# Kernel optimization log

Measured on AMD Instinct MI355X. Metric: run time of the kernel, lower is better.

Reference implementation:

```python
import jax, jax.numpy as jnp
import numpy as np

E = 128  # embedding_dim
C = 32   # per-head dim
H = 4    # heads
L = 256  # seq_len
N = 1    # batch


def layer_norm(x, gamma, beta, eps=1e-5):
    mu = jnp.mean(x, axis=-1, keepdims=True)
    var = jnp.mean((x - mu) ** 2, axis=-1, keepdims=True)
    return (x - mu) * jax.lax.rsqrt(var + eps) * gamma + beta


def setup_inputs() -> dict:
    key = jax.random.key(0)
    ks = jax.random.split(key, 12)
    s = E ** -0.5
    return {
        "pair_rep": jax.random.normal(ks[0], (N, L, L, E), dtype=jnp.float32),
        "mask": jax.random.normal(ks[1], (N, L, L), dtype=jnp.float32) * 0.1,
        "gamma": jnp.ones((E,), dtype=jnp.float32),
        "beta": jnp.zeros((E,), dtype=jnp.float32),
        "Wq": jax.random.normal(ks[2], (E, C * H), dtype=jnp.float32) * s,
        "Wk": jax.random.normal(ks[3], (E, C * H), dtype=jnp.float32) * s,
        "Wv": jax.random.normal(ks[4], (E, C * H), dtype=jnp.float32) * s,
        "Wb": jax.random.normal(ks[5], (E, H), dtype=jnp.float32) * s,
        "Wfu": jax.random.normal(ks[6], (E, C * H), dtype=jnp.float32) * s,
        "bfu": jnp.zeros((C * H,), dtype=jnp.float32),
        "Wo": jax.random.normal(ks[7], (C * H, E), dtype=jnp.float32) * (C * H) ** -0.5,
        "bo": jnp.zeros((E,), dtype=jnp.float32),
    }


def reference(pair_rep, mask, gamma, beta, Wq, Wk, Wv, Wb, Wfu, bfu, Wo, bo):
    n, s, _, _ = pair_rep.shape
    x = layer_norm(pair_rep, gamma, beta)  # [n,s,s,E]
    q = (x @ Wq).reshape(n, s, s, H, C) * (C ** -0.5)
    k = (x @ Wk).reshape(n, s, s, H, C)
    v = (x @ Wv).reshape(n, s, s, H, C)
    # faithful to original einsum: keys carry the q index, queries the v index
    dpa = jnp.einsum('nsqhc,nsvhc->nsqvh', k, q)  # [n,s,q,v,h]
    dpa = dpa + mask[:, None, :, :, None]
    pair_bias = x @ Wb  # [n,s,s,H]
    attn = jax.nn.softmax(dpa + pair_bias[:, None], axis=3)
    out = jnp.einsum('nsqvh,nsvhc->nsqhc', attn, v)  # [n,s,q,h,c]
    fu = jax.nn.sigmoid(x @ Wfu + bfu).reshape(n, s, s, H, C)
    out = out * fu
    out = out.reshape(n, s, s, H * C) @ Wo + bo
    return out
```

## Files before the change

kernel.cpp:

```cpp
#include <hip/hip_runtime.h>
#include <math.h>

#define L 256
#define E 128
#define H 4
#define C 32
#define P (L*L)

typedef __bf16 bf16;
typedef __bf16 bf16x8 __attribute__((ext_vector_type(8)));
typedef __bf16 bf16x4 __attribute__((ext_vector_type(4)));
typedef float  f32x4  __attribute__((ext_vector_type(4)));

#define MFMA(a,b,c) __builtin_amdgcn_mfma_f32_16x16x32_bf16((a),(b),(c),0,0,0)

__global__ __launch_bounds__(256) void k_prep(
    const float* __restrict__ Wq, const float* __restrict__ Wk,
    const float* __restrict__ Wv, const float* __restrict__ Wfu,
    const float* __restrict__ Wo, const float* __restrict__ Wb,
    bf16* __restrict__ WF, bf16* __restrict__ WoF, bf16* __restrict__ WbF)
{
  const int b = blockIdx.x;
  const int lane = threadIdx.x & 63, wv = threadIdx.x >> 6;
  const int g = lane >> 4, l15 = lane & 15;
  if (b < 40) {
    const int m = b >> 3;
    const int f = (b & 7) * 4 + wv;
    const float* W = (m==0)?Wq:(m==1)?Wk:(m==2)?Wv:(m==3)?Wfu:Wo;
    bf16* dst = (m < 4) ? (WF + (size_t)m * 16384) : WoF;
    const float sc = (m == 0) ? 0.17677669529663689f : 1.0f;
    const int mt = f >> 2, kt = f & 3;
    const int row = 16*mt + l15, k0 = 32*kt + 8*g;
    bf16x8 o;
    #pragma unroll
    for (int j = 0; j < 8; ++j) o[j] = (bf16)(W[(size_t)(k0+j)*128 + row] * sc);
    *(bf16x8*)(dst + ((size_t)f*64 + lane)*8) = o;
  } else {
    const int kt = wv, k0 = 32*kt + 8*g;
    bf16x8 o;
    #pragma unroll
    for (int j = 0; j < 8; ++j)
      o[j] = (l15 < 4) ? (bf16)Wb[(size_t)(k0+j)*4 + l15] : (bf16)0.0f;
    *(bf16x8*)(WbF + ((size_t)kt*64 + lane)*8) = o;
  }
}

__global__ __launch_bounds__(512) void k_ln_proj(
    const float* __restrict__ pr, const float* __restrict__ gamma,
    const float* __restrict__ beta, const float* __restrict__ bfu,
    const bf16* __restrict__ WF, const bf16* __restrict__ WbF,
    bf16* __restrict__ qb, bf16* __restrict__ kb, bf16* __restrict__ vb,
    bf16* __restrict__ gfb, float* __restrict__ pbo)
{
  __shared__ bf16 xs[64 * 136];
  __shared__ bf16 stag[4][16 * 136];
  const int tid = threadIdx.x;
  const int base = blockIdx.x * 64;
  const int w = tid >> 6, lane = tid & 63, g = lane >> 4, l15 = lane & 15;
  const int m = w & 3, half = w >> 2;

  const bf16* WFw = WF + (size_t)m * 16384 + (size_t)half * 8192;
  f32x4 af[16];
  #pragma unroll
  for (int f = 0; f < 16; ++f)
    af[f] = *(const f32x4*)(WFw + ((size_t)f*64 + lane)*8);

  {
    const int pl = tid >> 3, sub = tid & 7;
    const float4* src = (const float4*)(pr + (size_t)(base + pl) * 128 + sub * 16);
    float4 r[4];
    float s = 0.f, ss = 0.f;
    #pragma unroll
    for (int j = 0; j < 4; ++j) {
      r[j] = src[j];
      s  += r[j].x + r[j].y + r[j].z + r[j].w;
      ss += r[j].x*r[j].x + r[j].y*r[j].y + r[j].z*r[j].z + r[j].w*r[j].w;
    }
    s  += __shfl_xor(s, 1, 8);  s  += __shfl_xor(s, 2, 8);  s  += __shfl_xor(s, 4, 8);
    ss += __shfl_xor(ss, 1, 8); ss += __shfl_xor(ss, 2, 8); ss += __shfl_xor(ss, 4, 8);
    const float mu   = s * 0.0078125f;
    const float var  = ss * 0.0078125f - mu * mu;
    const float rstd = rsqrtf(var + 1e-5f);
    const float4* g4 = (const float4*)(gamma + sub * 16);
    const float4* b4 = (const float4*)(beta + sub * 16);
    bf16* xr = xs + pl * 136 + sub * 16;
    #pragma unroll
    for (int i = 0; i < 2; ++i) {
      float4 r0 = r[2*i], r1 = r[2*i+1];
      float4 gg0 = g4[2*i], gg1 = g4[2*i+1], bb0 = b4[2*i], bb1 = b4[2*i+1];
      bf16x8 o;
      o[0] = (bf16)((r0.x - mu) * rstd * gg0.x + bb0.x);
      o[1] = (bf16)((r0.y - mu) * rstd * gg0.y + bb0.y);
      o[2] = (bf16)((r0.z - mu) * rstd * gg0.z + bb0.z);
      o[3] = (bf16)((r0.w - mu) * rstd * gg0.w + bb0.w);
      o[4] = (bf16)((r1.x - mu) * rstd * gg1.x + bb1.x);
      o[5] = (bf16)((r1.y - mu) * rstd * gg1.y + bb1.y);
      o[6] = (bf16)((r1.z - mu) * rstd * gg1.z + bb1.z);
      o[7] = (bf16)((r1.w - mu) * rstd * gg1.w + bb1.w);
      *(bf16x8*)(xr + 8 * i) = o;
    }
  }

  #pragma unroll
  for (int f = 0; f < 16; ++f)
    asm volatile("" : "+v"(af[f]));

  __syncthreads();

  const f32x4 z = {0.f, 0.f, 0.f, 0.f};

  if (w < 4) {
    f32x4 acc = z;
    #pragma unroll
    for (int kt = 0; kt < 4; ++kt) {
      bf16x8 a = *(const bf16x8*)(WbF + ((size_t)kt*64 + lane)*8);
      bf16x8 b = *(const bf16x8*)(xs + (16*w + l15)*136 + 32*kt + 8*g);
      acc = MFMA(a, b, acc);
    }
    if (g == 0)
      *(float4*)(pbo + (size_t)(base + 16*w + l15)*4) =
          make_float4(acc[0], acc[1], acc[2], acc[3]);
  }

  bf16* stw = stag[m];
  bf16* dst = (m == 0) ? qb : (m == 1) ? kb : (m == 2) ? vb : gfb;

  for (int nt = 0; nt < 4; ++nt) {
    bf16x8 bfr[4];
    #pragma unroll
    for (int kt = 0; kt < 4; ++kt)
      bfr[kt] = *(const bf16x8*)(xs + (16*nt + l15)*136 + 32*kt + 8*g);
    f32x4 acc[4];
    #pragma unroll
    for (int mtl = 0; mtl < 4; ++mtl) acc[mtl] = z;
    #pragma unroll
    for (int kt = 0; kt < 4; ++kt)
      #pragma unroll
      for (int mtl = 0; mtl < 4; ++mtl)
        acc[mtl] = MFMA(__builtin_bit_cast(bf16x8, af[mtl*4 + kt]), bfr[kt], acc[mtl]);

    #pragma unroll
    for (int mtl = 0; mtl < 4; ++mtl) {
      const int col = half*64 + 16*mtl + 4*g;
      f32x4 vv = acc[mtl];
      if (m == 3) {
        float4 bb = *(const float4*)(bfu + col);
        vv[0] = 1.f / (1.f + __expf(-(vv[0] + bb.x)));
        vv[1] = 1.f / (1.f + __expf(-(vv[1] + bb.y)));
        vv[2] = 1.f / (1.f + __expf(-(vv[2] + bb.z)));
        vv[3] = 1.f / (1.f + __expf(-(vv[3] + bb.w)));
      }
      bf16x4 o;
      o[0] = (bf16)vv[0]; o[1] = (bf16)vv[1]; o[2] = (bf16)vv[2]; o[3] = (bf16)vv[3];
      *(bf16x4*)(stw + l15*136 + col) = o;
    }

    #pragma unroll
    for (int i = 0; i < 2; ++i) {
      const int flat = i*512 + lane*8;
      const int p = flat >> 6, cf = half*64 + (flat & 63);
      bf16x8 val = *(const bf16x8*)(stw + p*136 + cf);
      *(bf16x8*)(dst + ((size_t)(base + 16*nt + p))*128 + cf) = val;
    }
  }
}

__global__ __launch_bounds__(256) void k_bias(
    const float* __restrict__ mask, const float* __restrict__ pb,
    bf16* __restrict__ T5)
{
  const int q = blockIdx.x;
  const int v = threadIdx.x;
  const size_t qv = (size_t)q*256 + v;
  const float m = mask[qv];
  float4 p = *(const float4*)(pb + qv*4);
  T5[qv]            = (bf16)(m + p.x);
  T5[qv +   65536]  = (bf16)(m + p.y);
  T5[qv + 2*65536]  = (bf16)(m + p.z);
  T5[qv + 3*65536]  = (bf16)(m + p.w);
}

__global__ __launch_bounds__(512) void k_attn(
    const bf16* __restrict__ qb, const bf16* __restrict__ kb,
    const bf16* __restrict__ vb, const bf16* __restrict__ T5,
    bf16* __restrict__ aob)
{
  __shared__ bf16 qs[256 * 40];
  __shared__ bf16 vT[32 * 264];
  const int tid = threadIdx.x;
  const int s = blockIdx.x >> 2, h = blockIdx.x & 3;
  const int rb = s * 256;
  const int hc = 32 * h;
  const bf16* T5h = T5 + (size_t)h * 65536;

  const int w = tid >> 6, lane = tid & 63, g = lane >> 4, l15 = lane & 15;

  #pragma unroll
  for (int i = 0; i < 2; ++i) {
    const int flat = i*4096 + tid*8;
    const int pos = flat >> 5, cc = flat & 31;
    const int slot = (pos & 0xE3) | ((pos & 0x04) << 2) | ((pos & 0x18) >> 1);
    bf16x8 qv = *(const bf16x8*)(qb + ((size_t)rb + pos)*128 + hc + cc);
    *(bf16x8*)(qs + slot*40 + cc) = qv;
    bf16x8 vv = *(const bf16x8*)(vb + ((size_t)rb + pos)*128 + hc + cc);
    #pragma unroll
    for (int j = 0; j < 8; ++j) {
      const int row = cc + j;
      const int a = row >> 3;
      const int X = (a << 5) | ((a >> 1) << 4);
      vT[row*264 + (pos ^ X)] = vv[j];
    }
  }

  bf16x8 bq0 = *(const bf16x8*)(kb + ((size_t)rb + w*32 +      l15)*128 + hc + 8*g);
  bf16x8 bq1 = *(const bf16x8*)(kb + ((size_t)rb + w*32 + 16 + l15)*128 + hc + 8*g);

  __syncthreads();

  bf16x8 av[2][8];
  #pragma unroll
  for (int mt = 0; mt < 2; ++mt) {
    const int row = 16*mt + l15;
    const int a = row >> 3;
    const int X = (a << 5) | ((a >> 1) << 4);
    #pragma unroll
    for (int kt = 0; kt < 8; ++kt)
      av[mt][kt] = *(const bf16x8*)(vT + row*264 + ((32*kt + 8*g) ^ X));
  }

  const f32x4 z = {0.f, 0.f, 0.f, 0.f};

  #pragma unroll
  for (int qt = 0; qt < 2; ++qt) {
    const int q = w*32 + qt*16 + l15;
    const bf16x8 bq = qt ? bq1 : bq0;
    const bf16* Trow = T5h + (size_t)q * 256 + 8*g;
    f32x4 o0a = z, o0b = z, o1a = z, o1b = z;
    float rs = 0.f;
    #pragma unroll
    for (int kt = 0; kt < 8; ++kt) {
      bf16x8 a0 = *(const bf16x8*)(qs + (16*(2*kt + 0) + l15)*40 + 8*g);
      bf16x8 a1 = *(const bf16x8*)(qs + (16*(2*kt + 1) + l15)*40 + 8*g);
      f32x4 s0 = MFMA(a0, bq, z);
      f32x4 s1 = MFMA(a1, bq, z);
      bf16x4 b0 = *(const bf16x4*)(Trow + 32*kt);
      bf16x4 b1 = *(const bf16x4*)(Trow + 32*kt + 4);
      bf16x8 pf;
      #pragma unroll
      for (int r = 0; r < 4; ++r) {
        float e0 = __expf(s0[r] + (float)b0[r]);
        float e1 = __expf(s1[r] + (float)b1[r]);
        pf[r]     = (bf16)e0;
        pf[4 + r] = (bf16)e1;
        rs += e0 + e1;
      }
      if (kt & 1) {
        o0b = MFMA(av[0][kt], pf, o0b);
        o1b = MFMA(av[1][kt], pf, o1b);
      } else {
        o0a = MFMA(av[0][kt], pf, o0a);
        o1a = MFMA(av[1][kt], pf, o1a);
      }
    }
    rs += __shfl_xor(rs, 16);
    rs += __shfl_xor(rs, 32);
    const float inv = 1.f / rs;
    bf16x4 p0, p1;
    #pragma unroll
    for (int r = 0; r < 4; ++r) {
      p0[r] = (bf16)((o0a[r] + o0b[r]) * inv);
      p1[r] = (bf16)((o1a[r] + o1b[r]) * inv);
    }
    bf16* dst = aob + ((size_t)rb + q)*128 + hc;
    *(bf16x4*)(dst + 4*g)      = p0;
    *(bf16x4*)(dst + 16 + 4*g) = p1;
  }
}

__global__ __launch_bounds__(512) void k_gate_out(
    const bf16* __restrict__ aob, const bf16* __restrict__ gfb,
    const bf16* __restrict__ WoF, const float* __restrict__ bo,
    float* __restrict__ out)
{
  __shared__ bf16 gs[64 * 136];
  const int tid = threadIdx.x;
  const int base = blockIdx.x * 64;
  const int w = tid >> 6, lane = tid & 63, g = lane >> 4, l15 = lane & 15;

  f32x4 wf[4];
  #pragma unroll
  for (int kt = 0; kt < 4; ++kt)
    wf[kt] = *(const f32x4*)(WoF + ((size_t)(w*4 + kt)*64 + lane)*8);

  #pragma unroll
  for (int i = 0; i < 2; ++i) {
    const int flat = i*4096 + tid*8;
    const int pos = flat >> 7, c = flat & 127;
    const size_t off = (size_t)(base + pos)*128 + c;
    bf16x8 a = *(const bf16x8*)(aob + off);
    bf16x8 f = *(const bf16x8*)(gfb + off);
    bf16x8 o;
    #pragma unroll
    for (int j = 0; j < 8; ++j) o[j] = (bf16)((float)a[j] * (float)f[j]);
    *(bf16x8*)(gs + pos*136 + c) = o;
  }

  #pragma unroll
  for (int kt = 0; kt < 4; ++kt)
    asm volatile("" : "+v"(wf[kt]));

  __syncthreads();

  const f32x4 z = {0.f, 0.f, 0.f, 0.f};
  const int col = 16*w + 4*g;
  const float4 bb = *(const float4*)(bo + col);

  for (int nt = 0; nt < 4; ++nt) {
    bf16x8 bfr[4];
    #pragma unroll
    for (int kt = 0; kt < 4; ++kt)
      bfr[kt] = *(const bf16x8*)(gs + (16*nt + l15)*136 + 32*kt + 8*g);
    f32x4 a0 = z;
    #pragma unroll
    for (int kt = 0; kt < 4; ++kt)
      a0 = MFMA(__builtin_bit_cast(bf16x8, wf[kt]), bfr[kt], a0);
    const int pos = base + 16*nt + l15;
    *(float4*)(out + (size_t)pos*128 + col) =
        make_float4(a0[0] + bb.x, a0[1] + bb.y, a0[2] + bb.z, a0[3] + bb.w);
  }
}

extern "C" void kernel_launch(void* const* d_in, const int* in_sizes, int n_in,
                              void* d_out, int out_size, void* d_ws, size_t ws_size,
                              hipStream_t stream) {
  const float* pr    = (const float*)d_in[0];
  const float* mask  = (const float*)d_in[1];
  const float* gamma = (const float*)d_in[2];
  const float* beta  = (const float*)d_in[3];
  const float* Wq    = (const float*)d_in[4];
  const float* Wk    = (const float*)d_in[5];
  const float* Wv    = (const float*)d_in[6];
  const float* Wb    = (const float*)d_in[7];
  const float* Wfu   = (const float*)d_in[8];
  const float* bfu   = (const float*)d_in[9];
  const float* Wo    = (const float*)d_in[10];
  const float* bo    = (const float*)d_in[11];
  float* out = (float*)d_out;

  bf16* qb  = (bf16*)d_ws;
  bf16* kb  = qb  + (size_t)P * 128;
  bf16* vb  = kb  + (size_t)P * 128;
  bf16* gfb = vb  + (size_t)P * 128;
  bf16* aob = gfb + (size_t)P * 128;
  bf16* T5  = aob + (size_t)P * 128;
  bf16* WF  = T5  + (size_t)H * P;
  bf16* WoF = WF  + 4 * 16384;
  bf16* WbF = WoF + 16384;
  float* pb = (float*)(WbF + 2048);

  k_prep<<<41, 256, 0, stream>>>(Wq, Wk, Wv, Wfu, Wo, Wb, WF, WoF, WbF);
  k_ln_proj<<<1024, 512, 0, stream>>>(pr, gamma, beta, bfu, WF, WbF,
                                      qb, kb, vb, gfb, pb);
  k_bias<<<256, 256, 0, stream>>>(mask, pb, T5);
  k_attn<<<1024, 512, 0, stream>>>(qb, kb, vb, T5, aob);
  k_gate_out<<<1024, 512, 0, stream>>>(aob, gfb, WoF, bo, out);
}
```

Baseline: 168.0 us.

## Fuse mask-bias add into projection kernel and stage attention output via LDS

```diff
diff --git a/kernel.cpp b/kernel.cpp
--- a/kernel.cpp
+++ b/kernel.cpp
@@ -49,8 +49,9 @@
     const float* __restrict__ pr, const float* __restrict__ gamma,
     const float* __restrict__ beta, const float* __restrict__ bfu,
     const bf16* __restrict__ WF, const bf16* __restrict__ WbF,
+    const float* __restrict__ mask,
     bf16* __restrict__ qb, bf16* __restrict__ kb, bf16* __restrict__ vb,
-    bf16* __restrict__ gfb, float* __restrict__ pbo)
+    bf16* __restrict__ gfb, bf16* __restrict__ T5)
 {
   __shared__ bf16 xs[64 * 136];
   __shared__ bf16 stag[4][16 * 136];
@@ -117,9 +118,14 @@
       bf16x8 b = *(const bf16x8*)(xs + (16*w + l15)*136 + 32*kt + 8*g);
       acc = MFMA(a, b, acc);
     }
-    if (g == 0)
-      *(float4*)(pbo + (size_t)(base + 16*w + l15)*4) =
-          make_float4(acc[0], acc[1], acc[2], acc[3]);
+    if (g == 0) {
+      const int pos = base + 16*w + l15;
+      const float mv = mask[pos];
+      T5[pos]            = (bf16)(mv + acc[0]);
+      T5[pos +   65536]  = (bf16)(mv + acc[1]);
+      T5[pos + 2*65536]  = (bf16)(mv + acc[2]);
+      T5[pos + 3*65536]  = (bf16)(mv + acc[3]);
+    }
   }
 
   bf16* stw = stag[m];
@@ -165,21 +171,6 @@
   }
 }
 
-__global__ __launch_bounds__(256) void k_bias(
-    const float* __restrict__ mask, const float* __restrict__ pb,
-    bf16* __restrict__ T5)
-{
-  const int q = blockIdx.x;
-  const int v = threadIdx.x;
-  const size_t qv = (size_t)q*256 + v;
-  const float m = mask[qv];
-  float4 p = *(const float4*)(pb + qv*4);
-  T5[qv]            = (bf16)(m + p.x);
-  T5[qv +   65536]  = (bf16)(m + p.y);
-  T5[qv + 2*65536]  = (bf16)(m + p.z);
-  T5[qv + 3*65536]  = (bf16)(m + p.w);
-}
-
 __global__ __launch_bounds__(512) void k_attn(
     const bf16* __restrict__ qb, const bf16* __restrict__ kb,
     const bf16* __restrict__ vb, const bf16* __restrict__ T5,
@@ -227,6 +218,9 @@
     for (int kt = 0; kt < 8; ++kt)
       av[mt][kt] = *(const bf16x8*)(vT + row*264 + ((32*kt + 8*g) ^ X));
   }
+
+  __syncthreads();
+  bf16* aost = vT;
 
   const f32x4 z = {0.f, 0.f, 0.f, 0.f};
 
@@ -271,9 +265,20 @@
       p0[r] = (bf16)((o0a[r] + o0b[r]) * inv);
       p1[r] = (bf16)((o1a[r] + o1b[r]) * inv);
     }
-    bf16* dst = aob + ((size_t)rb + q)*128 + hc;
+    bf16* dst = aost + (size_t)q * 32;
     *(bf16x4*)(dst + 4*g)      = p0;
     *(bf16x4*)(dst + 16 + 4*g) = p1;
+  }
+
+  __syncthreads();
+
+  bf16* aoh = aob + (size_t)h * P * 32;
+  #pragma unroll
+  for (int i = 0; i < 2; ++i) {
+    const int flat = i*4096 + tid*8;
+    const int pos = flat >> 5, cc = flat & 31;
+    *(bf16x8*)(aoh + ((size_t)rb + pos)*32 + cc) =
+        *(const bf16x8*)(aost + pos*32 + cc);
   }
 }
 
@@ -295,10 +300,9 @@
   #pragma unroll
   for (int i = 0; i < 2; ++i) {
     const int flat = i*4096 + tid*8;
-    const int pos = flat >> 7, c = flat & 127;
-    const size_t off = (size_t)(base + pos)*128 + c;
-    bf16x8 a = *(const bf16x8*)(aob + off);
-    bf16x8 f = *(const bf16x8*)(gfb + off);
+    const int pos = flat >> 7, c = flat & 127, h = c >> 5;
+    bf16x8 a = *(const bf16x8*)(aob + ((size_t)h*P + base + pos)*32 + (c & 31));
+    bf16x8 f = *(const bf16x8*)(gfb + ((size_t)(base + pos))*128 + c);
     bf16x8 o;
     #pragma unroll
     for (int j = 0; j < 8; ++j) o[j] = (bf16)((float)a[j] * (float)f[j]);
@@ -356,12 +360,10 @@
   bf16* WF  = T5  + (size_t)H * P;
   bf16* WoF = WF  + 4 * 16384;
   bf16* WbF = WoF + 16384;
-  float* pb = (float*)(WbF + 2048);
 
   k_prep<<<41, 256, 0, stream>>>(Wq, Wk, Wv, Wfu, Wo, Wb, WF, WoF, WbF);
-  k_ln_proj<<<1024, 512, 0, stream>>>(pr, gamma, beta, bfu, WF, WbF,
-                                      qb, kb, vb, gfb, pb);
-  k_bias<<<256, 256, 0, stream>>>(mask, pb, T5);
+  k_ln_proj<<<1024, 512, 0, stream>>>(pr, gamma, beta, bfu, WF, WbF, mask,
+                                      qb, kb, vb, gfb, T5);
   k_attn<<<1024, 512, 0, stream>>>(qb, kb, vb, T5, aob);
   k_gate_out<<<1024, 512, 0, stream>>>(aob, gfb, WoF, bo, out);
 }
```

Result: slower. 173.4 us (+3.2%).
